# Performance work log

Hardware: AMD Instinct MI355X
Metric: run time of the kernel (lower is better)

The kernel has to match this reference:

```python
import jax, jax.numpy as jnp
import numpy as np

B, S, E, H = 4, 2048, 1024, 16
D = E // H  # head dim = 64


def setup_inputs() -> dict:
    key = jax.random.key(0)
    ks = jax.random.split(key, 9)
    sc = 1.0 / np.sqrt(E)
    x = jax.random.normal(ks[0], (B, S, E), dtype=jnp.float32)
    # causal mask: 1 = keep, 0 = masked -> -inf (matches masked_fill(mask==0, -inf))
    mask = jnp.broadcast_to(jnp.tril(jnp.ones((S, S), dtype=jnp.int32)), (B, S, S))
    return {
        "x": x,
        "mask": mask,
        "wq": jax.random.normal(ks[1], (E, E), dtype=jnp.float32) * sc,
        "bq": jax.random.normal(ks[2], (E,), dtype=jnp.float32) * sc,
        "wk": jax.random.normal(ks[3], (E, E), dtype=jnp.float32) * sc,
        "bk": jax.random.normal(ks[4], (E,), dtype=jnp.float32) * sc,
        "wv": jax.random.normal(ks[5], (E, E), dtype=jnp.float32) * sc,
        "bv": jax.random.normal(ks[6], (E,), dtype=jnp.float32) * sc,
        "wo": jax.random.normal(ks[7], (E, E), dtype=jnp.float32) * sc,
        "bo": jax.random.normal(ks[8], (E,), dtype=jnp.float32) * sc,
    }


def reference(x, mask, wq, bq, wk, bk, wv, bv, wo, bo):
    # nn.Linear: y = x @ W^T + b
    def proj(w, b):
        y = jnp.einsum('bse,fe->bsf', x, w) + b
        return y.reshape(B, S, H, D).transpose(0, 2, 1, 3)  # [B,H,S,D]

    q = proj(wq, bq)
    k = proj(wk, bk)
    v = proj(wv, bv)
    denom = jnp.asarray(np.sqrt(D), dtype=x.dtype)
    score = jnp.einsum('bhqd,bhkd->bhqk', q, k) / denom  # [B,H,S,S]
    score = jnp.where(mask[:, None, :, :] == 0, jnp.asarray(-jnp.inf, score.dtype), score)
    attn = jax.nn.softmax(score, axis=-1)
    out = jnp.einsum('bhqk,bhkd->bhqd', attn, v)  # [B,H,S,D]
    out = out.transpose(0, 2, 1, 3).reshape(B, S, E)
    return jnp.einsum('bse,fe->bsf', out, wo) + bo
```

## Files before the change

kernel.cpp:

```cpp
#include <hip/hip_runtime.h>
#include <cstdint>
#include <cstddef>

typedef unsigned short u16;
typedef __bf16 bf16;
typedef bf16 bf16x8 __attribute__((ext_vector_type(8)));
typedef bf16 bf16x4 __attribute__((ext_vector_type(4)));
typedef float f32x4 __attribute__((ext_vector_type(4)));
typedef u16 u16x8 __attribute__((ext_vector_type(8)));
typedef u16 u16x4 __attribute__((ext_vector_type(4)));

#define ASYNC16(g, l) __builtin_amdgcn_global_load_lds( \
    (const __attribute__((address_space(1))) void*)(g), \
    (__attribute__((address_space(3))) void*)(l), 16, 0, 0)

#define FENCE asm volatile("" ::: "memory")
#define BARRIER do { FENCE; __builtin_amdgcn_s_barrier(); FENCE; } while (0)
#define WAITVM(n) asm volatile("s_waitcnt vmcnt(" #n ")" ::: "memory")

__device__ __forceinline__ u16 f2bf(float f) {
  bf16 h = (bf16)f;
  return __builtin_bit_cast(u16, h);
}

__device__ __forceinline__ u16x4 pk4(float a, float b, float c, float d) {
  bf16x4 v = { (bf16)a, (bf16)b, (bf16)c, (bf16)d };
  return __builtin_bit_cast(u16x4, v);
}

__device__ __forceinline__ void store_out(u16* p, float v) { *p = f2bf(v); }
__device__ __forceinline__ void store_out(float* p, float v) { *p = v; }

__device__ __forceinline__ f32x4 mfma16(bf16x8 a, bf16x8 b, f32x4 c) {
  return __builtin_amdgcn_mfma_f32_16x16x32_bf16(a, b, c, 0, 0, 0);
}

__global__ void prep(const float* __restrict__ x,  const float* __restrict__ wq,
                     const float* __restrict__ wk, const float* __restrict__ wv,
                     const float* __restrict__ wo, const float* __restrict__ bq,
                     const float* __restrict__ bk,
                     u16* __restrict__ xb, u16* __restrict__ wqkb,
                     u16* __restrict__ wvb, u16* __restrict__ wob,
                     float* __restrict__ bqk, float scl)
{
  const int bid = blockIdx.x, tid = threadIdx.x;
  if (bid < 8192) {
    int i = bid * 256 + tid;
    float4 v = ((const float4*)x)[i];
    ((u16x4*)xb)[i] = pk4(v.x, v.y, v.z, v.w);
  } else if (bid < 12288) {
    int wsel = (bid - 8192) >> 10;
    int i = ((bid - 8192) & 1023) * 256 + tid;
    const float* src = wsel == 0 ? wq : wsel == 1 ? wk : wsel == 2 ? wv : wo;
    u16* dst = wsel == 0 ? wqkb : wsel == 1 ? wqkb + 1048576 : wsel == 2 ? wvb : wob;
    float s = wsel == 0 ? scl : 1.0f;
    float4 v = ((const float4*)src)[i];
    ((u16x4*)dst)[i] = pk4(v.x * s, v.y * s, v.z * s, v.w * s);
  } else {
    for (int i = tid; i < 1024; i += 256) {
      bqk[i] = bq[i] * scl;
      bqk[1024 + i] = bk[i];
    }
  }
}

template <typename OutT>
__device__ __forceinline__ void gemm256(
    u16* sA, u16* sB,
    const u16* __restrict__ A, const u16* __restrict__ Bm,
    const float* __restrict__ bias_col, const float* __restrict__ bias_row,
    OutT* __restrict__ C, int M, int N, int K, int bm, int bn)
{
  const int tid = threadIdx.x;
  const int w = tid >> 6, lane = tid & 63;
  const int quad = lane >> 4, l15 = lane & 15;
  const int wr = w >> 2, wc = w & 3;

  const int srow = tid >> 3;
  const int sslot = (tid & 7) ^ (srow & 7);
  const u16* gA = A + (size_t)(bm * 256 + srow) * K + sslot * 8;
  const u16* gB = Bm + (size_t)(bn * 256 + srow) * K + sslot * 8;
  u16* dA = sA + tid * 8;
  u16* dB = sB + tid * 8;
  const size_t rK64 = (size_t)64 * K, rK128 = (size_t)128 * K;

  auto stageA = [&](int c, int h, int kt) {
    const u16* s = gA + h * rK128 + kt * 64;
    u16* d = dA + c * 16384 + h * 8192;
    ASYNC16(s, d);
    ASYNC16(s + rK64, d + 4096);
  };
  auto stageB = [&](int c, int h, int kt) {
    const u16* s = gB + h * rK128 + kt * 64;
    u16* d = dB + c * 16384 + h * 8192;
    ASYNC16(s, d);
    ASYNC16(s + rK64, d + 4096);
  };

  f32x4 acc[8][4] = {};
  bf16x8 af[4][2];
  bf16x8 bf0[2][2];
  bf16x8 bf1[2][2];

  const int aRow = (wr * 128 + l15) * 64;
  const int bRow = (wc * 64 + l15) * 64;
  const int sw0 = (quad ^ (l15 & 7)) * 8;

#define LDA8(SRC, MH) do { \
    _Pragma("unroll") \
    for (int i = 0; i < 4; i++) { \
      af[i][0] = *(const bf16x8*)((SRC) + aRow + ((MH)*4 + i) * 1024 + sw0); \
      af[i][1] = *(const bf16x8*)((SRC) + aRow + ((MH)*4 + i) * 1024 + (sw0 ^ 32)); \
    } } while (0)

#define LDB4(DST, SRC, NH) do { \
    _Pragma("unroll") \
    for (int j = 0; j < 2; j++) { \
      DST[j][0] = *(const bf16x8*)((SRC) + bRow + ((NH)*2 + j) * 1024 + sw0); \
      DST[j][1] = *(const bf16x8*)((SRC) + bRow + ((NH)*2 + j) * 1024 + (sw0 ^ 32)); \
    } } while (0)

#define MMQ(MH, NH, BF) do { \
    __builtin_amdgcn_s_setprio(1); \
    _Pragma("unroll") \
    for (int i = 0; i < 4; i++) { \
      acc[(MH)*4+i][(NH)*2+0] = mfma16(af[i][0], BF[0][0], acc[(MH)*4+i][(NH)*2+0]); \
      acc[(MH)*4+i][(NH)*2+0] = mfma16(af[i][1], BF[0][1], acc[(MH)*4+i][(NH)*2+0]); \
      acc[(MH)*4+i][(NH)*2+1] = mfma16(af[i][0], BF[1][0], acc[(MH)*4+i][(NH)*2+1]); \
      acc[(MH)*4+i][(NH)*2+1] = mfma16(af[i][1], BF[1][1], acc[(MH)*4+i][(NH)*2+1]); \
    } \
    __builtin_amdgcn_s_setprio(0); \
  } while (0)

  const int NT = K >> 6, NI = NT >> 1;

  stageB(0, 0, 0); stageB(0, 1, 0);
  stageA(0, 0, 0); stageA(0, 1, 0);
  stageB(1, 0, 1); stageB(1, 1, 1);
  WAITVM(4);
  BARRIER;

  u16* sA0 = sA;         u16* sA1 = sA + 16384;
  u16* sB0 = sB;         u16* sB1 = sB + 16384;

  for (int t = 0; t < NI; ++t) {
    const int k1 = 2 * t + 1, kn = 2 * t + 2, kn1 = 2 * t + 3;
    const bool more = (t + 1 < NI);

    LDA8(sA0, 0); LDB4(bf0, sB0, 0);
    stageA(1, 0, k1);
    BARRIER;
    MMQ(0, 0, bf0);
    BARRIER;

    LDB4(bf1, sB0, 1);
    stageA(1, 1, k1);
    BARRIER;
    MMQ(0, 1, bf1);
    BARRIER;

    LDA8(sA0, 1);
    if (more) stageB(0, 0, kn);
    BARRIER;
    MMQ(1, 1, bf1);
    BARRIER;

    if (more) { stageB(0, 1, kn); WAITVM(4); }
    else      { WAITVM(0); }
    BARRIER;
    MMQ(1, 0, bf0);
    BARRIER;

    LDA8(sA1, 0); LDB4(bf0, sB1, 0);
    if (more) stageA(0, 0, kn);
    BARRIER;
    MMQ(0, 0, bf0);
    BARRIER;

    LDB4(bf1, sB1, 1);
    if (more) stageA(0, 1, kn);
    BARRIER;
    MMQ(0, 1, bf1);
    BARRIER;

    LDA8(sA1, 1);
    if (more) stageB(1, 0, kn1);
    BARRIER;
    MMQ(1, 1, bf1);
    BARRIER;

    if (more) { stageB(1, 1, kn1); WAITVM(4); }
    BARRIER;
    MMQ(1, 0, bf0);
    BARRIER;
  }

#pragma unroll
  for (int nt = 0; nt < 4; nt++) {
    const int cc = bn * 256 + wc * 64 + nt * 16 + l15;
    const float bc = bias_col ? bias_col[cc] : 0.f;
#pragma unroll
    for (int mt = 0; mt < 8; mt++) {
      const int r0 = bm * 256 + wr * 128 + mt * 16 + quad * 4;
      f32x4 v = acc[mt][nt];
#pragma unroll
      for (int ri = 0; ri < 4; ri++) {
        const float bb = bc + (bias_row ? bias_row[r0 + ri] : 0.f);
        store_out(&C[(size_t)(r0 + ri) * N + cc], v[ri] + bb);
      }
    }
  }
#undef LDA8
#undef LDB4
#undef MMQ
}

__global__ __launch_bounds__(512, 2) void gemm_qkv(
    const u16* __restrict__ xb, const u16* __restrict__ wqkb,
    const u16* __restrict__ wvb, const float* __restrict__ bqk,
    const float* __restrict__ bv, u16* __restrict__ qk, u16* __restrict__ vt)
{
  __shared__ __align__(16) u16 sA[2 * 16384];
  __shared__ __align__(16) u16 sB[2 * 16384];
  const int id = blockIdx.x;
  if (id < 256) {
    gemm256<u16>(sA, sB, xb, wqkb, bqk, nullptr, qk, 8192, 2048, 1024,
                 id >> 3, id & 7);
  } else {
    const int j = id - 256, s = j >> 3;
    gemm256<u16>(sA, sB, wvb, xb, nullptr, bv, vt, 1024, 8192, 1024,
                 s & 3, (j & 7) * 4 + (s >> 2));
  }
}

__global__ __launch_bounds__(512, 2) void gemm_out(
    const u16* __restrict__ ctx, const u16* __restrict__ wob,
    const float* __restrict__ bo, float* __restrict__ out)
{
  __shared__ __align__(16) u16 sA[2 * 16384];
  __shared__ __align__(16) u16 sB[2 * 16384];
  const int id = blockIdx.x, s = id >> 3;
  gemm256<float>(sA, sB, ctx, wob, bo, nullptr, out, 8192, 1024, 1024,
                 (id & 7) * 4 + (s >> 2), s & 3);
}

__global__ __launch_bounds__(512, 2) void fattn(
    const u16* __restrict__ QK, const u16* __restrict__ VT, u16* __restrict__ ctx)
{
  __shared__ u16 Kt[128 * 64];
  __shared__ u16 Vt[64 * 128];
  __shared__ u16 Pt[8 * 32 * 64];

  const int tid = threadIdx.x;
  const int w = tid >> 6, lane = tid & 63;
  const int quad = lane >> 4, l15 = lane & 15;
  const int bx = blockIdx.x, h = blockIdx.y, b = blockIdx.z;
  const int P8[8] = {7, 0, 6, 1, 5, 2, 4, 3};
  const int tq = (b & 2) ? 7 - P8[bx] : P8[bx];
  const int qbase = tq * 256 + w * 32;

  const int kr = tid >> 3, kc = (tid & 7) ^ (kr & 7);
  const int vr = tid >> 4, vc = (tid & 15) ^ (vr & 15);

  const u16* QKb = QK + (size_t)b * 2048 * 2048;
  const u16* Kg = QKb + 1024 + h * 64 + kc * 8;
  const u16* Vg = VT + (size_t)(h * 64) * 8192 + b * 2048 + vc * 8;

  u16* Pw = Pt + w * 2048;

  bf16x8 ones;
#pragma unroll
  for (int j = 0; j < 8; j++) ones[j] = (bf16)1.0f;

  bf16x8 qf[2][2];
#pragma unroll
  for (int mt = 0; mt < 2; mt++)
#pragma unroll
    for (int ks = 0; ks < 2; ks++)
      qf[mt][ks] = *(const bf16x8*)(QKb + (size_t)(qbase + mt * 16 + l15) * 2048 +
                                    h * 64 + ks * 32 + quad * 8);

  f32x4 oacc[4][2] = {};
  f32x4 lacc[2] = {};

  const int tmax = 2 * tq + 1;
  for (int t = 0; t <= tmax; t++) {
    __syncthreads();
#pragma unroll
    for (int s = 0; s < 2; s++) {
      ASYNC16(Kg + (size_t)(t * 128 + s * 64 + kr) * 2048, Kt + (s * 512 + w * 64) * 8);
      ASYNC16(Vg + (size_t)(s * 32 + vr) * 8192 + t * 128,  Vt + (s * 512 + w * 64) * 8);
    }
    __syncthreads();

    f32x4 st[2][8] = {};
#pragma unroll
    for (int ks = 0; ks < 2; ks++) {
      bf16x8 kf[8];
#pragma unroll
      for (int nt = 0; nt < 8; nt++) {
        int row = nt * 16 + l15;
        kf[nt] = *(const bf16x8*)(Kt + (row * 8 + ((ks * 4 + quad) ^ (row & 7))) * 8);
      }
#pragma unroll
      for (int nt = 0; nt < 8; nt++) {
        st[0][nt] = mfma16(kf[nt], qf[0][ks], st[0][nt]);
        st[1][nt] = mfma16(kf[nt], qf[1][ks], st[1][nt]);
      }
    }

    if (t >= 2 * tq) {
#pragma unroll
      for (int mt = 0; mt < 2; mt++) {
        const int qg = qbase + mt * 16 + l15;
#pragma unroll
        for (int nt = 0; nt < 8; nt++)
#pragma unroll
          for (int r = 0; r < 4; r++)
            if (t * 128 + nt * 16 + quad * 4 + r > qg) st[mt][nt][r] = -3e38f;
      }
    }
#pragma unroll
    for (int mt = 0; mt < 2; mt++)
#pragma unroll
      for (int nt = 0; nt < 8; nt++)
#pragma unroll
        for (int r = 0; r < 4; r++)
          st[mt][nt][r] = exp2f(st[mt][nt][r]);

#pragma unroll
    for (int hf = 0; hf < 2; hf++) {
#pragma unroll
      for (int mt = 0; mt < 2; mt++) {
        const int row = mt * 16 + l15;
#pragma unroll
        for (int n2 = 0; n2 < 4; n2++) {
          int nt = hf * 4 + n2;
          u16x4 pk = pk4(st[mt][nt][0], st[mt][nt][1], st[mt][nt][2], st[mt][nt][3]);
          int c = n2 * 2 + (quad >> 1);
          *(u16x4*)(Pw + (row << 6) + ((c ^ (row & 7)) << 3) + ((quad & 1) << 2)) = pk;
        }
      }
#pragma unroll
      for (int ks = 0; ks < 2; ks++) {
        const int c = ks * 4 + quad;
        bf16x8 pf0 = *(const bf16x8*)(Pw + (l15 << 6) + ((c ^ (l15 & 7)) << 3));
        bf16x8 pf1 = *(const bf16x8*)(Pw + ((16 + l15) << 6) + ((c ^ (l15 & 7)) << 3));
        lacc[0] = mfma16(ones, pf0, lacc[0]);
        lacc[1] = mfma16(ones, pf1, lacc[1]);
#pragma unroll
        for (int dt = 0; dt < 4; dt++) {
          int row = dt * 16 + l15;
          bf16x8 vf = *(const bf16x8*)(Vt + (row * 16 + ((hf * 8 + ks * 4 + quad) ^ (row & 15))) * 8);
          oacc[dt][0] = mfma16(vf, pf0, oacc[dt][0]);
          oacc[dt][1] = mfma16(vf, pf1, oacc[dt][1]);
        }
      }
    }
  }

#pragma unroll
  for (int mt = 0; mt < 2; mt++) {
    float rl = 1.0f / lacc[mt][0];
    size_t row = (size_t)b * 2048 + qbase + mt * 16 + l15;
#pragma unroll
    for (int dt = 0; dt < 4; dt++) {
      u16x4 o = pk4(oacc[dt][mt][0] * rl, oacc[dt][mt][1] * rl,
                    oacc[dt][mt][2] * rl, oacc[dt][mt][3] * rl);
      *(u16x4*)(ctx + row * 1024 + h * 64 + dt * 16 + quad * 4) = o;
    }
  }
}

extern "C" void kernel_launch(void* const* d_in, const int* in_sizes, int n_in,
                              void* d_out, int out_size, void* d_ws, size_t ws_size,
                              hipStream_t stream)
{
  const float* x  = (const float*)d_in[0];
  const float* wq = (const float*)d_in[2];
  const float* bq = (const float*)d_in[3];
  const float* wk = (const float*)d_in[4];
  const float* bk = (const float*)d_in[5];
  const float* wv = (const float*)d_in[6];
  const float* bv = (const float*)d_in[7];
  const float* wo = (const float*)d_in[8];
  const float* bo = (const float*)d_in[9];

  const float SCL = 0.125f * 1.44269504088896f;

  char* ws = (char*)d_ws;
  u16*   xb   = (u16*)(ws);
  u16*   ctx  = (u16*)(ws);
  u16*   wqkb = (u16*)(ws + 16777216);
  u16*   wvb  = (u16*)(ws + 20971520);
  u16*   wob  = (u16*)(ws + 23068672);
  float* bqk  = (float*)(ws + 25165824);
  u16*   qk   = (u16*)(ws + 25174016);
  u16*   vt   = (u16*)(ws + 58728448);
  float* out  = (float*)d_out;

  prep<<<12289, 256, 0, stream>>>(x, wq, wk, wv, wo, bq, bk,
                                  xb, wqkb, wvb, wob, bqk, SCL);

  gemm_qkv<<<384, 512, 0, stream>>>(xb, wqkb, wvb, bqk, bv, qk, vt);
  fattn<<<dim3(8, 16, 4), 512, 0, stream>>>(qk, vt, ctx);
  gemm_out<<<128, 512, 0, stream>>>(ctx, wob, bo, out);
}
```

Baseline: 326.9 us.

## Shrink GEMM tiles to 128x256 with triple-buffered LDS pipeline

Replaces the 256x256 GEMM tile with a 128x256 tile and changes the K-loop from a double-buffered two-step unrolled schedule to a three-stage ring buffer that prefetches two K-tiles ahead. This doubles the block count for the QKV and output projections (768 and 256 blocks) to fill more of the MI355X's CUs, and halves the accumulator register footprint. In exchange, each block does less reuse of the B tile per load, so global and LDS traffic per FLOP rise, and LDS use per block grows to 144 KB.

```diff
diff --git a/kernel.cpp b/kernel.cpp
--- a/kernel.cpp
+++ b/kernel.cpp
@@ -65,7 +65,7 @@
 }
 
 template <typename OutT>
-__device__ __forceinline__ void gemm256(
+__device__ __forceinline__ void gemm128(
     u16* sA, u16* sB,
     const u16* __restrict__ A, const u16* __restrict__ Bm,
     const float* __restrict__ bias_col, const float* __restrict__ bias_row,
@@ -78,140 +78,112 @@
 
   const int srow = tid >> 3;
   const int sslot = (tid & 7) ^ (srow & 7);
-  const u16* gA = A + (size_t)(bm * 256 + srow) * K + sslot * 8;
+  const u16* gA = A + (size_t)(bm * 128 + srow) * K + sslot * 8;
   const u16* gB = Bm + (size_t)(bn * 256 + srow) * K + sslot * 8;
   u16* dA = sA + tid * 8;
   u16* dB = sB + tid * 8;
-  const size_t rK64 = (size_t)64 * K, rK128 = (size_t)128 * K;
-
-  auto stageA = [&](int c, int h, int kt) {
-    const u16* s = gA + h * rK128 + kt * 64;
-    u16* d = dA + c * 16384 + h * 8192;
-    ASYNC16(s, d);
-    ASYNC16(s + rK64, d + 4096);
+  const size_t rK64 = (size_t)64 * K;
+
+  auto stage0 = [&](int c, int kt) {
+    const u16* a = gA + kt * 64;
+    u16* da = dA + c * 8192;
+    ASYNC16(a, da);
+    ASYNC16(a + rK64, da + 4096);
+    ASYNC16(gB + kt * 64, dB + c * 16384);
   };
-  auto stageB = [&](int c, int h, int kt) {
-    const u16* s = gB + h * rK128 + kt * 64;
-    u16* d = dB + c * 16384 + h * 8192;
-    ASYNC16(s, d);
-    ASYNC16(s + rK64, d + 4096);
+  auto stage1 = [&](int c, int kt) {
+    const u16* b = gB + kt * 64;
+    u16* db = dB + c * 16384;
+    ASYNC16(b + rK64,     db + 4096);
+    ASYNC16(b + 2 * rK64, db + 8192);
+    ASYNC16(b + 3 * rK64, db + 12288);
   };
 
-  f32x4 acc[8][4] = {};
+  f32x4 acc[4][4] = {};
   bf16x8 af[4][2];
-  bf16x8 bf0[2][2];
-  bf16x8 bf1[2][2];
-
-  const int aRow = (wr * 128 + l15) * 64;
+  bf16x8 bfr[2][2];
+
+  const int aRow = (wr * 64 + l15) * 64;
   const int bRow = (wc * 64 + l15) * 64;
   const int sw0 = (quad ^ (l15 & 7)) * 8;
 
-#define LDA8(SRC, MH) do { \
+#define LDA(SRC) do { \
     _Pragma("unroll") \
     for (int i = 0; i < 4; i++) { \
-      af[i][0] = *(const bf16x8*)((SRC) + aRow + ((MH)*4 + i) * 1024 + sw0); \
-      af[i][1] = *(const bf16x8*)((SRC) + aRow + ((MH)*4 + i) * 1024 + (sw0 ^ 32)); \
+      af[i][0] = *(const bf16x8*)((SRC) + aRow + i * 1024 + sw0); \
+      af[i][1] = *(const bf16x8*)((SRC) + aRow + i * 1024 + (sw0 ^ 32)); \
     } } while (0)
 
-#define LDB4(DST, SRC, NH) do { \
+#define LDB(SRC, NH) do { \
     _Pragma("unroll") \
     for (int j = 0; j < 2; j++) { \
-      DST[j][0] = *(const bf16x8*)((SRC) + bRow + ((NH)*2 + j) * 1024 + sw0); \
-      DST[j][1] = *(const bf16x8*)((SRC) + bRow + ((NH)*2 + j) * 1024 + (sw0 ^ 32)); \
+      bfr[j][0] = *(const bf16x8*)((SRC) + bRow + ((NH)*2 + j) * 1024 + sw0); \
+      bfr[j][1] = *(const bf16x8*)((SRC) + bRow + ((NH)*2 + j) * 1024 + (sw0 ^ 32)); \
     } } while (0)
 
-#define MMQ(MH, NH, BF) do { \
+#define MMQ(NH) do { \
     __builtin_amdgcn_s_setprio(1); \
     _Pragma("unroll") \
     for (int i = 0; i < 4; i++) { \
-      acc[(MH)*4+i][(NH)*2+0] = mfma16(af[i][0], BF[0][0], acc[(MH)*4+i][(NH)*2+0]); \
-      acc[(MH)*4+i][(NH)*2+0] = mfma16(af[i][1], BF[0][1], acc[(MH)*4+i][(NH)*2+0]); \
-      acc[(MH)*4+i][(NH)*2+1] = mfma16(af[i][0], BF[1][0], acc[(MH)*4+i][(NH)*2+1]); \
-      acc[(MH)*4+i][(NH)*2+1] = mfma16(af[i][1], BF[1][1], acc[(MH)*4+i][(NH)*2+1]); \
+      acc[i][(NH)*2+0] = mfma16(af[i][0], bfr[0][0], acc[i][(NH)*2+0]); \
+      acc[i][(NH)*2+0] = mfma16(af[i][1], bfr[0][1], acc[i][(NH)*2+0]); \
+      acc[i][(NH)*2+1] = mfma16(af[i][0], bfr[1][0], acc[i][(NH)*2+1]); \
+      acc[i][(NH)*2+1] = mfma16(af[i][1], bfr[1][1], acc[i][(NH)*2+1]); \
     } \
     __builtin_amdgcn_s_setprio(0); \
   } while (0)
 
-  const int NT = K >> 6, NI = NT >> 1;
-
-  stageB(0, 0, 0); stageB(0, 1, 0);
-  stageA(0, 0, 0); stageA(0, 1, 0);
-  stageB(1, 0, 1); stageB(1, 1, 1);
-  WAITVM(4);
+  const int NT = K >> 6;
+
+  stage0(0, 0); stage1(0, 0);
+  stage0(1, 1); stage1(1, 1);
+  WAITVM(6);
   BARRIER;
 
-  u16* sA0 = sA;         u16* sA1 = sA + 16384;
-  u16* sB0 = sB;         u16* sB1 = sB + 16384;
-
-  for (int t = 0; t < NI; ++t) {
-    const int k1 = 2 * t + 1, kn = 2 * t + 2, kn1 = 2 * t + 3;
-    const bool more = (t + 1 < NI);
-
-    LDA8(sA0, 0); LDB4(bf0, sB0, 0);
-    stageA(1, 0, k1);
+  for (int t = 0; t < NT; ++t) {
+    const int c = t % 3, c2 = (t + 2) % 3;
+    const bool more = (t + 2 < NT);
+    const u16* SA = sA + c * 8192;
+    const u16* SB = sB + c * 16384;
+
+    LDA(SA); LDB(SB, 0);
+    if (more) stage0(c2, t + 2);
     BARRIER;
-    MMQ(0, 0, bf0);
+    MMQ(0);
     BARRIER;
 
-    LDB4(bf1, sB0, 1);
-    stageA(1, 1, k1);
+    LDB(SB, 1);
+    if (more) {
+      stage1(c2, t + 2);
+      WAITVM(6);
+    } else if (t == NT - 2) {
+      WAITVM(0);
+    }
     BARRIER;
-    MMQ(0, 1, bf1);
+    MMQ(1);
     BARRIER;
-
-    LDA8(sA0, 1);
-    if (more) stageB(0, 0, kn);
-    BARRIER;
-    MMQ(1, 1, bf1);
-    BARRIER;
-
-    if (more) { stageB(0, 1, kn); WAITVM(4); }
-    else      { WAITVM(0); }
-    BARRIER;
-    MMQ(1, 0, bf0);
-    BARRIER;
-
-    LDA8(sA1, 0); LDB4(bf0, sB1, 0);
-    if (more) stageA(0, 0, kn);
-    BARRIER;
-    MMQ(0, 0, bf0);
-    BARRIER;
-
-    LDB4(bf1, sB1, 1);
-    if (more) stageA(0, 1, kn);
-    BARRIER;
-    MMQ(0, 1, bf1);
-    BARRIER;
-
-    LDA8(sA1, 1);
-    if (more) stageB(1, 0, kn1);
-    BARRIER;
-    MMQ(1, 1, bf1);
-    BARRIER;
-
-    if (more) { stageB(1, 1, kn1); WAITVM(4); }
-    BARRIER;
-    MMQ(1, 0, bf0);
-    BARRIER;
-  }
-
-#pragma unroll
-  for (int nt = 0; nt < 4; nt++) {
-    const int cc = bn * 256 + wc * 64 + nt * 16 + l15;
-    const float bc = bias_col ? bias_col[cc] : 0.f;
-#pragma unroll
-    for (int mt = 0; mt < 8; mt++) {
-      const int r0 = bm * 256 + wr * 128 + mt * 16 + quad * 4;
-      f32x4 v = acc[mt][nt];
-#pragma unroll
-      for (int ri = 0; ri < 4; ri++) {
-        const float bb = bc + (bias_row ? bias_row[r0 + ri] : 0.f);
-        store_out(&C[(size_t)(r0 + ri) * N + cc], v[ri] + bb);
-      }
-    }
-  }
-#undef LDA8
-#undef LDB4
+  }
+
+#pragma unroll
+  for (int nh = 0; nh < 2; nh++) {
+#pragma unroll
+    for (int j = 0; j < 2; j++) {
+      const int cc = bn * 256 + wc * 64 + nh * 32 + j * 16 + l15;
+      const float bc = bias_col ? bias_col[cc] : 0.f;
+#pragma unroll
+      for (int i = 0; i < 4; i++) {
+        const int r0 = bm * 128 + wr * 64 + i * 16 + quad * 4;
+        f32x4 v = acc[i][nh * 2 + j];
+#pragma unroll
+        for (int ri = 0; ri < 4; ri++) {
+          const float bb = bc + (bias_row ? bias_row[r0 + ri] : 0.f);
+          store_out(&C[(size_t)(r0 + ri) * N + cc], v[ri] + bb);
+        }
+      }
+    }
+  }
+#undef LDA
+#undef LDB
 #undef MMQ
 }
 
@@ -220,16 +192,16 @@
     const u16* __restrict__ wvb, const float* __restrict__ bqk,
     const float* __restrict__ bv, u16* __restrict__ qk, u16* __restrict__ vt)
 {
-  __shared__ __align__(16) u16 sA[2 * 16384];
-  __shared__ __align__(16) u16 sB[2 * 16384];
+  __shared__ __align__(16) u16 sA[3 * 8192];
+  __shared__ __align__(16) u16 sB[3 * 16384];
   const int id = blockIdx.x;
-  if (id < 256) {
-    gemm256<u16>(sA, sB, xb, wqkb, bqk, nullptr, qk, 8192, 2048, 1024,
+  if (id < 512) {
+    gemm128<u16>(sA, sB, xb, wqkb, bqk, nullptr, qk, 8192, 2048, 1024,
                  id >> 3, id & 7);
   } else {
-    const int j = id - 256, s = j >> 3;
-    gemm256<u16>(sA, sB, wvb, xb, nullptr, bv, vt, 1024, 8192, 1024,
-                 s & 3, (j & 7) * 4 + (s >> 2));
+    const int j = id - 512;
+    gemm128<u16>(sA, sB, wvb, xb, nullptr, bv, vt, 1024, 8192, 1024,
+                 j & 7, j >> 3);
   }
 }
 
@@ -237,11 +209,11 @@
     const u16* __restrict__ ctx, const u16* __restrict__ wob,
     const float* __restrict__ bo, float* __restrict__ out)
 {
-  __shared__ __align__(16) u16 sA[2 * 16384];
-  __shared__ __align__(16) u16 sB[2 * 16384];
-  const int id = blockIdx.x, s = id >> 3;
-  gemm256<float>(sA, sB, ctx, wob, bo, nullptr, out, 8192, 1024, 1024,
-                 (id & 7) * 4 + (s >> 2), s & 3);
+  __shared__ __align__(16) u16 sA[3 * 8192];
+  __shared__ __align__(16) u16 sB[3 * 16384];
+  const int id = blockIdx.x;
+  gemm128<float>(sA, sB, ctx, wob, bo, nullptr, out, 8192, 1024, 1024,
+                 id >> 2, id & 3);
 }
 
 __global__ __launch_bounds__(512, 2) void fattn(
@@ -402,7 +374,7 @@
   prep<<<12289, 256, 0, stream>>>(x, wq, wk, wv, wo, bq, bk,
                                   xb, wqkb, wvb, wob, bqk, SCL);
 
-  gemm_qkv<<<384, 512, 0, stream>>>(xb, wqkb, wvb, bqk, bv, qk, vt);
+  gemm_qkv<<<768, 512, 0, stream>>>(xb, wqkb, wvb, bqk, bv, qk, vt);
   fattn<<<dim3(8, 16, 4), 512, 0, stream>>>(qk, vt, ctx);
-  gemm_out<<<128, 512, 0, stream>>>(ctx, wob, bo, out);
-}
+  gemm_out<<<256, 512, 0, stream>>>(ctx, wob, bo, out);
+}
```

Result: faster. 312.4 us (-4.4%).
